# Kernel optimization log

Measured on AMD Instinct MI355X. Metric: run time of the kernel, lower is better.

## Reference

```python
import jax, jax.numpy as jnp
import numpy as np

HEADS = 4


def rel_to_abs(x):
    """Convert relative logits [..., L, 2L-1] to absolute [..., L, L].
    out[..., i, j] = x[..., i, j - i + L - 1]."""
    L = x.shape[-2]
    idx = jnp.arange(L)[None, :] - jnp.arange(L)[:, None] + (L - 1)  # [L, L]
    idx = jnp.broadcast_to(idx, x.shape[:-1] + (L,))
    return jnp.take_along_axis(x, idx, axis=-1)


def setup_inputs() -> dict:
    key = jax.random.key(0)
    ks = jax.random.split(key, 5)
    b, c, h, w = 2, 256, 64, 64
    dh = c // HEADS
    return {
        "x": jax.random.normal(ks[0], (b, c, h, w), jnp.float32),
        "w_qkv": jax.random.normal(ks[1], (3 * c, c), jnp.float32) / np.float32(np.sqrt(c)),
        "w_out": jax.random.normal(ks[2], (c, c), jnp.float32) / np.float32(np.sqrt(c)),
        "rel_height": jax.random.normal(ks[3], (2 * h - 1, dh), jnp.float32),
        "rel_width": jax.random.normal(ks[4], (2 * w - 1, dh), jnp.float32),
    }


def reference(x, w_qkv, w_out, rel_height, rel_width):
    b, c, h, w = x.shape
    dh = c // HEADS
    N = h * w
    scale = dh ** -0.5

    # 1x1 conv == per-pixel matmul over channels
    qkv = jnp.einsum('bchw,oc->bohw', x, w_qkv)  # [b, 3c, h, w]
    q, k, v = jnp.split(qkv, 3, axis=1)

    def to_heads(t):  # [b, c, h, w] -> [b, H, N, dh]
        return t.reshape(b, HEADS, dh, N).transpose(0, 1, 3, 2)

    q = to_heads(q) * scale
    k = to_heads(k)
    v = to_heads(v)

    # content-content scores over spatial positions
    content = jnp.einsum('bnid,bnjd->bnij', q, k)  # [b, H, N, N]

    q5 = q.reshape(b, HEADS, h, w, dh)  # [b, H, x, y, dh]
    # width relative logits: [b,H,x,y,2w-1] -> abs -> [b,H,x,y,jw]
    rw = rel_to_abs(jnp.einsum('bnxyd,rd->bnxyr', q5, rel_width))
    # height relative logits on transposed spatial: [b,H,y,x,2h-1] -> [b,H,y,x,jh]
    rh = rel_to_abs(jnp.einsum('bnyxd,rd->bnyxr', q5.transpose(0, 1, 3, 2, 4), rel_height))

    logits = content.reshape(b, HEADS, h, w, h, w)
    logits = logits + rw[:, :, :, :, None, :]  # broadcast width bias over target height jh
    logits = logits + rh.transpose(0, 1, 3, 2, 4)[:, :, :, :, :, None]  # [b,H,x,y,jh] over jw

    attn = jax.nn.softmax(logits.reshape(b, HEADS, N, N), axis=-1)
    out = jnp.einsum('bnij,bnjd->bnid', attn, v)  # [b, H, N, dh]
    out = out.transpose(0, 1, 3, 2).reshape(b, c, h, w)
    out = jnp.einsum('bchw,oc->bohw', out, w_out)  # 1x1 out projection
    return out + x
```

## Files before the change

### kernel.cpp

```cpp
#include <hip/hip_runtime.h>

typedef unsigned short u16;
typedef unsigned int u32;
typedef __bf16 bf16x8 __attribute__((ext_vector_type(8)));
typedef __bf16 bf16x2 __attribute__((ext_vector_type(2)));
typedef float f32x4 __attribute__((ext_vector_type(4)));
typedef float f32x2 __attribute__((ext_vector_type(2)));
typedef u32 u32x4 __attribute__((ext_vector_type(4)));
typedef u32 u32x2 __attribute__((ext_vector_type(2)));

#define DEVI __device__ __forceinline__

#if defined(__has_builtin)
#if __has_builtin(__builtin_amdgcn_exp2f)
#define EXP2F(x) __builtin_amdgcn_exp2f(x)
#endif
#endif
#ifndef EXP2F
#define EXP2F(x) exp2f(x)
#endif

#define MFMA16(a, b, c) __builtin_amdgcn_mfma_f32_16x16x32_bf16(a, b, c, 0, 0, 0)

typedef __attribute__((address_space(1))) u32 gu32;
typedef __attribute__((address_space(3))) u32 lu32;
DEVI void gll16(const u16* g, u16* l) {
    __builtin_amdgcn_global_load_lds((const gu32*)g, (lu32*)l, 16, 0, 0);
}
#define WAIT_VM0() __builtin_amdgcn_s_waitcnt(0x0f70)

DEVI u16 f2bf(float f) {
    u32 u = __builtin_bit_cast(u32, f);
    u = (u + 0x7FFFu + ((u >> 16) & 1u)) >> 16;
    return (u16)u;
}
DEVI float bf2f(u16 h) {
    u32 u = ((u32)h) << 16;
    return __builtin_bit_cast(float, u);
}
DEVI float bfhi(u32 u) { return __builtin_bit_cast(float, u & 0xFFFF0000u); }
DEVI float bflo(u32 u) { return __builtin_bit_cast(float, u << 16); }
DEVI bf16x8 bc8(u32x4 u) { return __builtin_bit_cast(bf16x8, u); }
DEVI u32 pack2(float a, float b) {
    f32x2 v = {a, b};
    bf16x2 h = __builtin_convertvector(v, bf16x2);
    return __builtin_bit_cast(u32, h);
}

#define QSCALE 0.18033688011112042f

__global__ __launch_bounds__(256) void k_prep(const float* __restrict__ x,
                                              const float* __restrict__ wq,
                                              const float* __restrict__ wo,
                                              const float* __restrict__ relh,
                                              const float* __restrict__ relw,
                                              u16* __restrict__ xt, u16* __restrict__ wqb,
                                              u16* __restrict__ wob, u16* __restrict__ relhb,
                                              u16* __restrict__ relwb) {
    int bid = blockIdx.x;
    int t = threadIdx.x;
    if (bid < 512) {
        int pm = bid & 63, cm = (bid >> 6) & 3, b = bid >> 8;
        int p0 = pm * 64, c0 = cm * 64;
        __shared__ float tile[64][65];
#pragma unroll
        for (int it = 0; it < 4; ++it) {
            int idx = it * 256 + t;
            int cl = idx >> 4, f4 = idx & 15;
            f32x4 v = *(const f32x4*)(x + ((size_t)(b * 256 + c0 + cl)) * 4096 + p0 + f4 * 4);
            tile[cl][f4 * 4 + 0] = v[0];
            tile[cl][f4 * 4 + 1] = v[1];
            tile[cl][f4 * 4 + 2] = v[2];
            tile[cl][f4 * 4 + 3] = v[3];
        }
        __syncthreads();
#pragma unroll
        for (int it = 0; it < 2; ++it) {
            int idx = it * 256 + t;
            int pl = idx >> 3, g = idx & 7;
            u32x4 pk;
            pk.x = pack2(tile[g * 8 + 0][pl], tile[g * 8 + 1][pl]);
            pk.y = pack2(tile[g * 8 + 2][pl], tile[g * 8 + 3][pl]);
            pk.z = pack2(tile[g * 8 + 4][pl], tile[g * 8 + 5][pl]);
            pk.w = pack2(tile[g * 8 + 6][pl], tile[g * 8 + 7][pl]);
            *(u32x4*)(xt + ((size_t)(b * 4096 + p0 + pl)) * 256 + c0 + g * 8) = pk;
        }
    } else {
        int i0 = (bid - 512) * 256 + t;
#pragma unroll
        for (int i = i0; i < 196608; i += 65536) wqb[i] = f2bf(wq[i]);
        if (i0 < 65536) wob[i0] = f2bf(wo[i0]);
        if (i0 < 8192) {
            relhb[i0] = (i0 < 8128) ? f2bf(relh[i0]) : (u16)0;
            relwb[i0] = (i0 < 8128) ? f2bf(relw[i0]) : (u16)0;
        }
    }
}

__global__ __launch_bounds__(256) void k_qkv(const u16* __restrict__ xt, const u16* __restrict__ wqb,
                                             const u16* __restrict__ relwb,
                                             const u16* __restrict__ relhb,
                                             u16* __restrict__ q, u16* __restrict__ k,
                                             u16* __restrict__ vt, u16* __restrict__ Wabs,
                                             u16* __restrict__ HabsT) {
    int pm = blockIdx.x, on = blockIdx.y, b = blockIdx.z;
    int p0 = pm * 64, o0 = on * 64;
    __shared__ __align__(16) u16 Sm[64 * 256];
    int t = threadIdx.x;
    int wv = t >> 6, l = t & 63, quad = l >> 4, li = l & 15;

    u32x4 areg[8];
    const u32x4* arow = (const u32x4*)(xt + ((size_t)(b * 4096 + p0 + wv * 16 + li)) * 256);
#pragma unroll
    for (int kc = 0; kc < 8; ++kc) areg[kc] = arow[kc * 4 + quad];

    {
        int pc = l & 31;
#pragma unroll
        for (int i = 0; i < 8; ++i) {
            int r = wv * 16 + i * 2 + (l >> 5);
            gll16(wqb + (size_t)(o0 + r) * 256 + ((pc + r) & 31) * 8,
                  Sm + (wv * 16 + i * 2) * 256);
        }
    }
    WAIT_VM0();
    __syncthreads();

    f32x4 acc[4] = {{0, 0, 0, 0}, {0, 0, 0, 0}, {0, 0, 0, 0}, {0, 0, 0, 0}};
#pragma unroll
    for (int kc = 0; kc < 8; ++kc) {
        bf16x8 a = bc8(areg[kc]);
#pragma unroll
        for (int ct = 0; ct < 4; ++ct) {
            bf16x8 bb = bc8(*(const u32x4*)(Sm + (ct * 16 + li) * 256 +
                                            (((kc * 4 + quad) - (ct * 16 + li)) & 31) * 8));
            acc[ct] = MFMA16(a, bb, acc[ct]);
        }
    }

    int tensor = on >> 2, head = on & 3;
    if (tensor == 2) {
        __syncthreads();
        u16* T = Sm;
#pragma unroll
        for (int ct = 0; ct < 4; ++ct)
#pragma unroll
            for (int r = 0; r < 4; ++r)
                T[(ct * 16 + li) * 72 + wv * 16 + quad * 4 + r] = f2bf(acc[ct][r]);
        __syncthreads();
        int dr = t >> 2, pc = (t & 3) * 16;
        u32x4* g = (u32x4*)(vt + ((size_t)((b * 4 + head) * 64 + dr)) * 4096 + p0 + pc);
        const u32x4* s2 = (const u32x4*)(T + dr * 72 + pc);
        g[0] = s2[0];
        g[1] = s2[1];
    } else {
        u16* outp = (tensor == 0) ? q : k;
        float sc = (tensor == 0) ? QSCALE : 1.0f;
#pragma unroll
        for (int ct = 0; ct < 4; ++ct)
#pragma unroll
            for (int r = 0; r < 4; ++r) {
                int p = p0 + wv * 16 + quad * 4 + r;
                int d = ct * 16 + li;
                outp[((size_t)((b * 4 + head) * 4096 + p)) * 64 + d] = f2bf(acc[ct][r] * sc);
            }
        if (tensor == 0) {
            int bh = b * 4 + head;
            u16* T = Sm;
            u16* Ls = Sm + 64 * 72;
            __syncthreads();
#pragma unroll
            for (int ct = 0; ct < 4; ++ct)
#pragma unroll
                for (int r = 0; r < 4; ++r)
                    T[(wv * 16 + quad * 4 + r) * 72 + ct * 16 + li] = f2bf(acc[ct][r] * QSCALE);
            {
                int row = t >> 1, half = t & 1;
                const u32x4* g2 = (const u32x4*)(relwb + row * 64 + half * 32);
                u32x4* s2 = (u32x4*)(Ls + row * 72 + half * 32);
#pragma unroll
                for (int kk = 0; kk < 4; ++kk) s2[kk] = g2[kk];
            }
            __syncthreads();
            u32x4 aq2[2];
            aq2[0] = *(const u32x4*)(T + (wv * 16 + li) * 72 + quad * 8);
            aq2[1] = *(const u32x4*)(T + (wv * 16 + li) * 72 + 32 + quad * 8);

            f32x4 acc2[8];
#pragma unroll
            for (int ct = 0; ct < 8; ++ct) acc2[ct] = (f32x4){0.f, 0.f, 0.f, 0.f};
#pragma unroll
            for (int kc = 0; kc < 2; ++kc) {
                bf16x8 a = bc8(aq2[kc]);
#pragma unroll
                for (int ct = 0; ct < 8; ++ct) {
                    bf16x8 bb = bc8(*(const u32x4*)(Ls + (ct * 16 + li) * 72 + kc * 32 + quad * 8));
                    acc2[ct] = MFMA16(a, bb, acc2[ct]);
                }
            }
#pragma unroll
            for (int ct = 0; ct < 8; ++ct)
#pragma unroll
                for (int r = 0; r < 4; ++r) {
                    int row = wv * 16 + quad * 4 + r;
                    int j = (ct * 16 + li) - 63 + row;
                    if (j >= 0 && j < 64)
                        Wabs[((size_t)(bh * 4096 + p0 + row)) * 64 + j] = f2bf(acc2[ct][r]);
                }
            __syncthreads();
            {
                int row = t >> 1, half = t & 1;
                const u32x4* g2 = (const u32x4*)(relhb + row * 64 + half * 32);
                u32x4* s2 = (u32x4*)(Ls + row * 72 + half * 32);
#pragma unroll
                for (int kk = 0; kk < 4; ++kk) s2[kk] = g2[kk];
            }
            __syncthreads();
#pragma unroll
            for (int ct = 0; ct < 8; ++ct) acc2[ct] = (f32x4){0.f, 0.f, 0.f, 0.f};
#pragma unroll
            for (int kc = 0; kc < 2; ++kc) {
                bf16x8 a = bc8(aq2[kc]);
#pragma unroll
                for (int ct = 0; ct < 8; ++ct) {
                    bf16x8 bb = bc8(*(const u32x4*)(Ls + (ct * 16 + li) * 72 + kc * 32 + quad * 8));
                    acc2[ct] = MFMA16(a, bb, acc2[ct]);
                }
            }
            u16* Ht = Sm;
#pragma unroll
            for (int ct = 0; ct < 8; ++ct)
#pragma unroll
                for (int r = 0; r < 4; ++r) {
                    int row = wv * 16 + quad * 4 + r;
                    int j = (ct * 16 + li) - 63 + pm;
                    if (j >= 0 && j < 64) Ht[j * 72 + row] = f2bf(acc2[ct][r]);
                }
            __syncthreads();
            {
                int jr = t >> 2, pc2 = (t & 3) * 16;
                u32x4* g2 = (u32x4*)(HabsT + ((size_t)(bh * 64 + jr)) * 4096 + p0 + pc2);
                const u32x4* s2 = (const u32x4*)(Ht + jr * 72 + pc2);
                g2[0] = s2[0];
                g2[1] = s2[1];
            }
        }
    }
}

__global__ __launch_bounds__(256, 2) void k_flash(const u16* __restrict__ q,
                                                  const u16* __restrict__ kg,
                                                  const u16* __restrict__ vt,
                                                  const u16* __restrict__ Wabs,
                                                  const u16* __restrict__ HabsT,
                                                  u16* __restrict__ OP,
                                                  float* __restrict__ LS) {
    int pm = blockIdx.x, bh = blockIdx.y, ks = blockIdx.z;
    int p0 = pm * 256;
    __shared__ __align__(16) u16 Kt[2][64 * 64];
    __shared__ __align__(16) u16 Vl[2][64 * 64];
    int t = threadIdx.x, wv = t >> 6, l = t & 63, quad = l >> 4, li = l & 15;
    int rbase = wv * 64;

    u32x4 aq[4][2];
#pragma unroll
    for (int rs = 0; rs < 4; ++rs) {
        const u32x4* qrow =
            (const u32x4*)(q + ((size_t)(bh * 4096 + p0 + rbase + rs * 16 + li)) * 64);
        aq[rs][0] = qrow[quad];
        aq[rs][1] = qrow[4 + quad];
    }

    u32x2 wbp[4][4];
#pragma unroll
    for (int rs = 0; rs < 4; ++rs)
#pragma unroll
        for (int ct = 0; ct < 4; ++ct) {
            int jcol = ((ct >> 1) * 32) + quad * 8 + ((ct & 1) * 4);
            const u32* wp = (const u32*)(Wabs +
                                         ((size_t)(bh * 4096 + p0 + rbase + rs * 16 + li)) * 64 +
                                         jcol);
            wbp[rs][ct] = (u32x2){wp[0], wp[1]};
        }

    const u16* hbase = HabsT + ((size_t)(bh * 64 + ks * 16)) * 4096 + p0 + rbase;

    int ln3 = l >> 3, ln7 = l & 7;
    int xo = (ln7 ^ ln3) * 8;
    int R0 = wv * 8 + ln3, R1 = 32 + R0;
    int j0r = (R0 & 32) | ((R0 & 16) >> 2) | ((R0 & 8) << 1) | ((R0 & 4) << 1) | (R0 & 3);
    int j1r = (R1 & 32) | ((R1 & 16) >> 2) | ((R1 & 8) << 1) | ((R1 & 4) << 1) | (R1 & 3);
    const u16* kS0 = kg + ((size_t)(bh * 4096 + ks * 1024 + j0r)) * 64 + xo;
    const u16* kS1 = kg + ((size_t)(bh * 4096 + ks * 1024 + j1r)) * 64 + xo;
    const u16* vS0 = vt + ((size_t)(bh * 64 + R0)) * 4096 + ks * 1024 + xo;
    const u16* vS1 = vt + ((size_t)(bh * 64 + R1)) * 4096 + ks * 1024 + xo;
    int ldst = wv * 512;

    int o0 = li * 64 + ((quad ^ ln7) * 8);
    int o1 = li * 64 + (((quad + 4) ^ ln7) * 8);

    gll16(kS0, Kt[0] + ldst);
    gll16(kS1, Kt[0] + 2048 + ldst);
    gll16(vS0, Vl[0] + ldst);
    gll16(vS1, Vl[0] + 2048 + ldst);
    u16 hc[4];
#pragma unroll
    for (int rs = 0; rs < 4; ++rs) hc[rs] = hbase[rs * 16 + li];
    WAIT_VM0();

    f32x4 oacc[4][5];
#pragma unroll
    for (int rs = 0; rs < 4; ++rs)
#pragma unroll
        for (int ct = 0; ct < 5; ++ct) oacc[rs][ct] = (f32x4){0.f, 0.f, 0.f, 0.f};

    const u32x4 ones = {0x3F803F80u, 0x3F803F80u, 0x3F803F80u, 0x3F803F80u};

    for (int kt = 0; kt < 16; ++kt) {
        __syncthreads();
        int cur = kt & 1;
        const u16* Kc = Kt[cur];
        const u16* Vc = Vl[cur];
        u16 hn[4];
        if (kt < 15) {
            kS0 += 4096;
            kS1 += 4096;
            vS0 += 64;
            vS1 += 64;
            u16* Kn = Kt[cur ^ 1];
            u16* Vn = Vl[cur ^ 1];
            gll16(kS0, Kn + ldst);
            gll16(kS1, Kn + 2048 + ldst);
            gll16(vS0, Vn + ldst);
            gll16(vS1, Vn + 2048 + ldst);
#pragma unroll
            for (int rs = 0; rs < 4; ++rs) hn[rs] = hbase[(size_t)(kt + 1) * 4096 + rs * 16 + li];
        }

        u32x4 pf[4][2];
#pragma unroll
        for (int ct = 0; ct < 4; ++ct) {
            bf16x8 af0 = bc8(*(const u32x4*)(Kc + ct * 1024 + o0));
            bf16x8 af1 = bc8(*(const u32x4*)(Kc + ct * 1024 + o1));
#pragma unroll
            for (int rs = 0; rs < 4; ++rs) {
                float hh = bf2f(hc[rs]);
                u32x2 w = wbp[rs][ct];
                f32x4 s4 = {bflo(w.x) + hh, bfhi(w.x) + hh, bflo(w.y) + hh, bfhi(w.y) + hh};
                s4 = MFMA16(af0, bc8(aq[rs][0]), s4);
                s4 = MFMA16(af1, bc8(aq[rs][1]), s4);
                u32 pa = pack2(EXP2F(s4[0]), EXP2F(s4[1]));
                u32 pb = pack2(EXP2F(s4[2]), EXP2F(s4[3]));
                if (ct & 1) {
                    pf[rs][ct >> 1].z = pa;
                    pf[rs][ct >> 1].w = pb;
                } else {
                    pf[rs][ct >> 1].x = pa;
                    pf[rs][ct >> 1].y = pb;
                }
            }
        }

        __builtin_amdgcn_s_setprio(1);
#pragma unroll
        for (int dt = 0; dt < 4; ++dt) {
            bf16x8 B0 = bc8(*(const u32x4*)(Vc + dt * 1024 + o0));
            bf16x8 B1 = bc8(*(const u32x4*)(Vc + dt * 1024 + o1));
#pragma unroll
            for (int rs = 0; rs < 4; ++rs) {
                oacc[rs][dt] = MFMA16(bc8(pf[rs][0]), B0, oacc[rs][dt]);
                oacc[rs][dt] = MFMA16(bc8(pf[rs][1]), B1, oacc[rs][dt]);
            }
        }
#pragma unroll
        for (int rs = 0; rs < 4; ++rs) {
            oacc[rs][4] = MFMA16(bc8(pf[rs][0]), bc8(ones), oacc[rs][4]);
            oacc[rs][4] = MFMA16(bc8(pf[rs][1]), bc8(ones), oacc[rs][4]);
        }
        __builtin_amdgcn_s_setprio(0);

        if (kt < 15) {
            WAIT_VM0();
#pragma unroll
            for (int rs = 0; rs < 4; ++rs) hc[rs] = hn[rs];
        }
    }

#pragma unroll
    for (int rs = 0; rs < 4; ++rs) {
#pragma unroll
        for (int ct = 0; ct < 4; ++ct)
#pragma unroll
            for (int r = 0; r < 4; ++r) {
                int p = p0 + rbase + rs * 16 + quad * 4 + r;
                OP[((size_t)((ks * 8 + bh) * 4096 + p)) * 64 + ct * 16 + li] =
                    f2bf(oacc[rs][ct][r]);
            }
        if (li == 0) {
#pragma unroll
            for (int r = 0; r < 4; ++r) {
                int p = p0 + rbase + rs * 16 + quad * 4 + r;
                LS[(size_t)(ks * 8 + bh) * 4096 + p] = oacc[rs][4][r];
            }
        }
    }
}

__global__ __launch_bounds__(256) void k_out2(const u16* __restrict__ wob,
                                              const u16* __restrict__ OP,
                                              const float* __restrict__ LS,
                                              const float* __restrict__ x,
                                              float* __restrict__ out) {
    int pm = blockIdx.x, b = blockIdx.y, coh = blockIdx.z;
    int p0 = pm * 32;
    __shared__ __align__(16) u16 Bt[32 * 264];
    int t = threadIdx.x, wv = t >> 6, l = t & 63, quad = l >> 4, li = l & 15;

    {
        int row = t >> 3, head = (t >> 1) & 3, hf = t & 1;
        int bh = b * 4 + head;
        int p = p0 + row;
        const u32x4* o0p = (const u32x4*)(OP + ((size_t)(bh * 4096 + p)) * 64) + hf * 4;
        const u32x4* o1p = (const u32x4*)(OP + ((size_t)((8 + bh) * 4096 + p)) * 64) + hf * 4;
        const u32x4* o2p = (const u32x4*)(OP + ((size_t)((16 + bh) * 4096 + p)) * 64) + hf * 4;
        const u32x4* o3p = (const u32x4*)(OP + ((size_t)((24 + bh) * 4096 + p)) * 64) + hf * 4;
        float linv = 1.0f / (LS[(size_t)bh * 4096 + p] + LS[(size_t)(8 + bh) * 4096 + p] +
                             LS[(size_t)(16 + bh) * 4096 + p] + LS[(size_t)(24 + bh) * 4096 + p]);
        u16* dst = Bt + row * 264 + head * 64 + hf * 32;
#pragma unroll
        for (int kk = 0; kk < 4; ++kk) {
            u32x4 a = o0p[kk], c = o1p[kk], d = o2p[kk], e = o3p[kk];
            u32x4 pk;
            pk.x = pack2((bflo(a.x) + bflo(c.x) + bflo(d.x) + bflo(e.x)) * linv,
                         (bfhi(a.x) + bfhi(c.x) + bfhi(d.x) + bfhi(e.x)) * linv);
            pk.y = pack2((bflo(a.y) + bflo(c.y) + bflo(d.y) + bflo(e.y)) * linv,
                         (bfhi(a.y) + bfhi(c.y) + bfhi(d.y) + bfhi(e.y)) * linv);
            pk.z = pack2((bflo(a.z) + bflo(c.z) + bflo(d.z) + bflo(e.z)) * linv,
                         (bfhi(a.z) + bfhi(c.z) + bfhi(d.z) + bfhi(e.z)) * linv);
            pk.w = pack2((bflo(a.w) + bflo(c.w) + bflo(d.w) + bflo(e.w)) * linv,
                         (bfhi(a.w) + bfhi(c.w) + bfhi(d.w) + bfhi(e.w)) * linv);
            *(u32x4*)(dst + kk * 8) = pk;
        }
    }
    __syncthreads();

#pragma unroll
    for (int ci = 0; ci < 2; ++ci) {
        int com = coh * 2 + ci;
        int co0 = com * 64;
        f32x4 acc[2] = {{0, 0, 0, 0}, {0, 0, 0, 0}};
        const u32x4* arow = (const u32x4*)(wob + (size_t)(co0 + wv * 16 + li) * 256);
#pragma unroll
        for (int kc = 0; kc < 8; ++kc) {
            bf16x8 a = bc8(arow[kc * 4 + quad]);
#pragma unroll
            for (int ct = 0; ct < 2; ++ct) {
                bf16x8 bb = bc8(*(const u32x4*)(Bt + (ct * 16 + li) * 264 + kc * 32 + quad * 8));
                acc[ct] = MFMA16(a, bb, acc[ct]);
            }
        }
#pragma unroll
        for (int ct = 0; ct < 2; ++ct)
#pragma unroll
            for (int r = 0; r < 4; ++r) {
                size_t idx =
                    ((size_t)(b * 256 + co0 + wv * 16 + quad * 4 + r)) * 4096 + p0 + ct * 16 + li;
                out[idx] = acc[ct][r] + x[idx];
            }
    }
}

extern "C" void kernel_launch(void* const* d_in, const int* in_sizes, int n_in, void* d_out,
                              int out_size, void* d_ws, size_t ws_size, hipStream_t stream) {
    const float* x = (const float*)d_in[0];
    const float* wqkv = (const float*)d_in[1];
    const float* wout = (const float*)d_in[2];
    const float* relh = (const float*)d_in[3];
    const float* relw = (const float*)d_in[4];
    float* out = (float*)d_out;
    char* ws = (char*)d_ws;

    u16* xt = (u16*)(ws + 0);
    u16* wqb = (u16*)(ws + 4194304);
    u16* wob = (u16*)(ws + 4587520);
    u16* relwb = (u16*)(ws + 4718592);
    u16* relhb = (u16*)(ws + 4734976);
    u16* qb = (u16*)(ws + 4751360);
    u16* kb = (u16*)(ws + 8945664);
    u16* vtb = (u16*)(ws + 13139968);
    u16* Wabs = (u16*)(ws + 17334272);
    u16* HabsT = (u16*)(ws + 21528576);
    u16* OPart = (u16*)(ws + 25722880);
    float* LSum = (float*)(ws + 0);

    k_prep<<<768, 256, 0, stream>>>(x, wqkv, wout, relh, relw, xt, wqb, wob, relhb, relwb);
    k_qkv<<<dim3(64, 12, 2), 256, 0, stream>>>(xt, wqb, relwb, relhb, qb, kb, vtb, Wabs, HabsT);
    k_flash<<<dim3(16, 8, 4), 256, 0, stream>>>(qb, kb, vtb, Wabs, HabsT, OPart, LSum);
    k_out2<<<dim3(128, 2, 2), 256, 0, stream>>>(wob, OPart, LSum, x, out);
}
```

Measured before the change: 136.4 us.

## Process two key tiles per barrier with doubled LDS staging in flash kernel

The flash attention loop now loads two 64-key K/V tiles per phase into a larger double-buffered LDS region and iterates 8 phases instead of 16. This halves the number of __syncthreads barriers and vmcnt waits per block and issues larger batches of async global-to-LDS loads. In exchange, LDS use doubles to 64KB per block, which may reduce occupancy below the two blocks per CU requested by the launch bounds.

```diff
diff --git a/kernel.cpp b/kernel.cpp
--- a/kernel.cpp
+++ b/kernel.cpp
@@ -257,8 +257,8 @@
                                                   float* __restrict__ LS) {
     int pm = blockIdx.x, bh = blockIdx.y, ks = blockIdx.z;
     int p0 = pm * 256;
-    __shared__ __align__(16) u16 Kt[2][64 * 64];
-    __shared__ __align__(16) u16 Vl[2][64 * 64];
+    __shared__ __align__(16) u16 Kt[4 * 64 * 64];
+    __shared__ __align__(16) u16 Vl[4 * 64 * 64];
     int t = threadIdx.x, wv = t >> 6, l = t & 63, quad = l >> 4, li = l & 15;
     int rbase = wv * 64;
 
@@ -287,25 +287,29 @@
 
     int ln3 = l >> 3, ln7 = l & 7;
     int xo = (ln7 ^ ln3) * 8;
-    int R0 = wv * 8 + ln3, R1 = 32 + R0;
-    int j0r = (R0 & 32) | ((R0 & 16) >> 2) | ((R0 & 8) << 1) | ((R0 & 4) << 1) | (R0 & 3);
-    int j1r = (R1 & 32) | ((R1 & 16) >> 2) | ((R1 & 8) << 1) | ((R1 & 4) << 1) | (R1 & 3);
+    int R0 = wv * 8 + ln3;
+    int j0r = ((R0 & 16) >> 2) | ((R0 & 8) << 1) | ((R0 & 4) << 1) | (R0 & 3);
     const u16* kS0 = kg + ((size_t)(bh * 4096 + ks * 1024 + j0r)) * 64 + xo;
-    const u16* kS1 = kg + ((size_t)(bh * 4096 + ks * 1024 + j1r)) * 64 + xo;
     const u16* vS0 = vt + ((size_t)(bh * 64 + R0)) * 4096 + ks * 1024 + xo;
-    const u16* vS1 = vt + ((size_t)(bh * 64 + R1)) * 4096 + ks * 1024 + xo;
     int ldst = wv * 512;
 
     int o0 = li * 64 + ((quad ^ ln7) * 8);
     int o1 = li * 64 + (((quad + 4) ^ ln7) * 8);
 
-    gll16(kS0, Kt[0] + ldst);
-    gll16(kS1, Kt[0] + 2048 + ldst);
-    gll16(vS0, Vl[0] + ldst);
-    gll16(vS1, Vl[0] + 2048 + ldst);
-    u16 hc[4];
-#pragma unroll
-    for (int rs = 0; rs < 4; ++rs) hc[rs] = hbase[rs * 16 + li];
+    gll16(kS0, Kt + ldst);
+    gll16(kS0 + 2048, Kt + 2048 + ldst);
+    gll16(kS0 + 4096, Kt + 4096 + ldst);
+    gll16(kS0 + 6144, Kt + 6144 + ldst);
+    gll16(vS0, Vl + ldst);
+    gll16(vS0 + 32 * 4096, Vl + 2048 + ldst);
+    gll16(vS0 + 64, Vl + 4096 + ldst);
+    gll16(vS0 + 32 * 4096 + 64, Vl + 6144 + ldst);
+    u16 hcA[4], hcB[4];
+#pragma unroll
+    for (int rs = 0; rs < 4; ++rs) {
+        hcA[rs] = hbase[rs * 16 + li];
+        hcB[rs] = hbase[(size_t)4096 + rs * 16 + li];
+    }
     WAIT_VM0();
 
     f32x4 oacc[4][5];
@@ -316,35 +320,14 @@
 
     const u32x4 ones = {0x3F803F80u, 0x3F803F80u, 0x3F803F80u, 0x3F803F80u};
 
-    for (int kt = 0; kt < 16; ++kt) {
-        __syncthreads();
-        int cur = kt & 1;
-        const u16* Kc = Kt[cur];
-        const u16* Vc = Vl[cur];
-        u16 hn[4];
-        if (kt < 15) {
-            kS0 += 4096;
-            kS1 += 4096;
-            vS0 += 64;
-            vS1 += 64;
-            u16* Kn = Kt[cur ^ 1];
-            u16* Vn = Vl[cur ^ 1];
-            gll16(kS0, Kn + ldst);
-            gll16(kS1, Kn + 2048 + ldst);
-            gll16(vS0, Vn + ldst);
-            gll16(vS1, Vn + 2048 + ldst);
-#pragma unroll
-            for (int rs = 0; rs < 4; ++rs) hn[rs] = hbase[(size_t)(kt + 1) * 4096 + rs * 16 + li];
-        }
-
-        u32x4 pf[4][2];
+    auto QKf = [&](const u16* Kc, const u16* hq, u32x4 (&pf)[4][2]) {
 #pragma unroll
         for (int ct = 0; ct < 4; ++ct) {
             bf16x8 af0 = bc8(*(const u32x4*)(Kc + ct * 1024 + o0));
             bf16x8 af1 = bc8(*(const u32x4*)(Kc + ct * 1024 + o1));
 #pragma unroll
             for (int rs = 0; rs < 4; ++rs) {
-                float hh = bf2f(hc[rs]);
+                float hh = bf2f(hq[rs]);
                 u32x2 w = wbp[rs][ct];
                 f32x4 s4 = {bflo(w.x) + hh, bfhi(w.x) + hh, bflo(w.y) + hh, bfhi(w.y) + hh};
                 s4 = MFMA16(af0, bc8(aq[rs][0]), s4);
@@ -360,7 +343,8 @@
                 }
             }
         }
-
+    };
+    auto PVf = [&](const u32x4 (&pf)[4][2], const u16* Vc) {
         __builtin_amdgcn_s_setprio(1);
 #pragma unroll
         for (int dt = 0; dt < 4; ++dt) {
@@ -378,11 +362,47 @@
             oacc[rs][4] = MFMA16(bc8(pf[rs][1]), bc8(ones), oacc[rs][4]);
         }
         __builtin_amdgcn_s_setprio(0);
-
-        if (kt < 15) {
+    };
+
+    for (int ph = 0; ph < 8; ++ph) {
+        __syncthreads();
+        int hp = (ph & 1) * 2 * 4096;
+        const u16* KA = Kt + hp;
+        const u16* VA = Vl + hp;
+        u16 hn0[4], hn1[4];
+        if (ph < 7) {
+            kS0 += 8192;
+            vS0 += 128;
+            int np = (2 * 4096) - hp;
+            u16* Kn = Kt + np + ldst;
+            u16* Vn = Vl + np + ldst;
+            gll16(kS0, Kn);
+            gll16(kS0 + 2048, Kn + 2048);
+            gll16(kS0 + 4096, Kn + 4096);
+            gll16(kS0 + 6144, Kn + 6144);
+            gll16(vS0, Vn);
+            gll16(vS0 + 32 * 4096, Vn + 2048);
+            gll16(vS0 + 64, Vn + 4096);
+            gll16(vS0 + 32 * 4096 + 64, Vn + 6144);
+#pragma unroll
+            for (int rs = 0; rs < 4; ++rs) {
+                hn0[rs] = hbase[(size_t)(2 * ph + 2) * 4096 + rs * 16 + li];
+                hn1[rs] = hbase[(size_t)(2 * ph + 3) * 4096 + rs * 16 + li];
+            }
+        }
+
+        u32x4 pf[4][2];
+        QKf(KA, hcA, pf);
+        PVf(pf, VA);
+        QKf(KA + 4096, hcB, pf);
+        PVf(pf, VA + 4096 - 0 + (Vl - Kt) * 0);
+        if (ph < 7) {
             WAIT_VM0();
 #pragma unroll
-            for (int rs = 0; rs < 4; ++rs) hc[rs] = hn[rs];
+            for (int rs = 0; rs < 4; ++rs) {
+                hcA[rs] = hn0[rs];
+                hcB[rs] = hn1[rs];
+            }
         }
     }
 
```

Result: no change. 137.0 us (+0.4%).
